# Kernel tuning notes

Measured on AMD Instinct MI355X. Metric: run time of the kernel, lower is better.

Reference implementation:

```python
import jax, jax.numpy as jnp
import numpy as np

N_NODES = 100000
N_EDGES = 6400000
TOKEN_DIM = 16


def setup_inputs() -> dict:
    key = jax.random.key(0)
    k1, k2, k3, k4, k5 = jax.random.split(key, 5)
    x = jax.random.normal(k1, (N_NODES, 1), dtype=jnp.float32)
    edge_index = jax.random.randint(k2, (2, N_EDGES), 0, N_NODES, dtype=jnp.int64)
    # PyTorch nn.Linear init: U(-1/sqrt(fan_in), 1/sqrt(fan_in)); plain normals are fine for a correctness baseline
    w1 = jax.random.normal(k3, (TOKEN_DIM, 2), dtype=jnp.float32) * (1.0 / np.sqrt(2.0))
    b1 = jnp.zeros((TOKEN_DIM,), dtype=jnp.float32)
    w2 = jax.random.normal(k4, (TOKEN_DIM, TOKEN_DIM), dtype=jnp.float32) * (1.0 / np.sqrt(TOKEN_DIM))
    b2 = jnp.zeros((TOKEN_DIM,), dtype=jnp.float32)
    return {"x": x, "edge_index": edge_index, "w1": w1, "b1": b1, "w2": w2, "b2": b2}


def reference(x, edge_index, w1, b1, w2, b2):
    row, col = edge_index[0], edge_index[1]
    # gather-multiply: bond_e = s_row * s_col, shape [E, 1]
    bond = x[row] * x[col]
    # scatter-add into local_field, shape [N, 1]
    local_field = jax.ops.segment_sum(bond, row, num_segments=x.shape[0])
    feats = jnp.concatenate([x, local_field], axis=1)  # [N, 2]
    h = jax.nn.relu(feats @ w1.T + b1)                  # [N, token_dim]
    tokens = jax.nn.relu(h @ w2.T + b2)                 # [N, token_dim]
    return tokens
```

## Files before the change

kernel.cpp:

```cpp
#include <hip/hip_runtime.h>
#include <hip/hip_bf16.h>

#define TOKEN_DIM 16
#define RANGES 5
#define MAX_RS 20000
#define MAX_C  96
#define NXCD   8

__global__ __launch_bounds__(1024, 8)
void nit_phase1(const int* __restrict__ row, const int* __restrict__ col,
                const float* __restrict__ x,
                unsigned short* __restrict__ partial,
                int N, long long E, int chunkE, int RS, int C) {
    __shared__ float acc[MAX_RS];
    const int b = blockIdx.x;
    const int k = b % NXCD;
    const int s = b / NXCD;
    const int r = s % RANGES;
    const int c = k + NXCD * (s / RANGES);
    if (c >= C) return;

    const int base = r * RS;
    int cnt = N - base; if (cnt > RS) cnt = RS; if (cnt < 0) cnt = 0;
    const int t = threadIdx.x, nt = blockDim.x;

    for (int j = t; j < cnt; j += nt) acc[j] = 0.0f;
    __syncthreads();

    long long i0 = (long long)c * chunkE;
    long long i1 = i0 + chunkE; if (i1 > E) i1 = E;
    long long len = (i1 > i0) ? (i1 - i0) : 0;
    long long ngrp = len >> 3;

    long long g = t;
    int4 r0a, r1a, c0a, c1a;
    if (g < ngrp) {
        long long idx = i0 + (g << 3);
        r0a = *reinterpret_cast<const int4*>(row + idx);
        r1a = *reinterpret_cast<const int4*>(row + idx + 4);
        c0a = *reinterpret_cast<const int4*>(col + idx);
        c1a = *reinterpret_cast<const int4*>(col + idx + 4);
    }
    while (g < ngrp) {
        const long long gn = g + nt;
        int4 r0b, r1b, c0b, c1b;
        if (gn < ngrp) {
            long long idx = i0 + (gn << 3);
            r0b = *reinterpret_cast<const int4*>(row + idx);
            r1b = *reinterpret_cast<const int4*>(row + idx + 4);
            c0b = *reinterpret_cast<const int4*>(col + idx);
            c1b = *reinterpret_cast<const int4*>(col + idx + 4);
        }
        unsigned d;
        d = (unsigned)(r0a.x - base); if (d < (unsigned)cnt) atomicAdd(&acc[d], x[c0a.x]);
        d = (unsigned)(r0a.y - base); if (d < (unsigned)cnt) atomicAdd(&acc[d], x[c0a.y]);
        d = (unsigned)(r0a.z - base); if (d < (unsigned)cnt) atomicAdd(&acc[d], x[c0a.z]);
        d = (unsigned)(r0a.w - base); if (d < (unsigned)cnt) atomicAdd(&acc[d], x[c0a.w]);
        d = (unsigned)(r1a.x - base); if (d < (unsigned)cnt) atomicAdd(&acc[d], x[c1a.x]);
        d = (unsigned)(r1a.y - base); if (d < (unsigned)cnt) atomicAdd(&acc[d], x[c1a.y]);
        d = (unsigned)(r1a.z - base); if (d < (unsigned)cnt) atomicAdd(&acc[d], x[c1a.z]);
        d = (unsigned)(r1a.w - base); if (d < (unsigned)cnt) atomicAdd(&acc[d], x[c1a.w]);
        r0a = r0b; r1a = r1b; c0a = c0b; c1a = c1b;
        g = gn;
    }
    for (long long idx = i0 + (ngrp << 3) + t; idx < i1; idx += nt) {
        unsigned d = (unsigned)(row[idx] - base);
        if (d < (unsigned)cnt) atomicAdd(&acc[d], x[col[idx]]);
    }
    __syncthreads();

    unsigned short* dst = partial + (size_t)c * N + base;
    for (int j = t; j < cnt; j += nt) {
        __hip_bfloat16 h = __float2bfloat16(acc[j]);
        __builtin_nontemporal_store(*reinterpret_cast<unsigned short*>(&h), dst + j);
    }
}

__global__ __launch_bounds__(256, 8)
void nit_phase2(const float* __restrict__ x,
                const unsigned short* __restrict__ partial,
                const float* __restrict__ w1, const float* __restrict__ b1,
                const float* __restrict__ w2, const float* __restrict__ b2,
                float* __restrict__ out, int N, int C) {
    __shared__ float sw1[TOKEN_DIM * 2];
    __shared__ float sb1[TOKEN_DIM];
    __shared__ float sw2[TOKEN_DIM * TOKEN_DIM];
    __shared__ float sb2[TOKEN_DIM];
    __shared__ float red[256];

    const int t = threadIdx.x;
    if (t < TOKEN_DIM * TOKEN_DIM) sw2[t] = w2[t];
    if (t < TOKEN_DIM * 2) sw1[t] = w1[t];
    if (t < TOKEN_DIM) { sb1[t] = b1[t]; sb2[t] = b2[t]; }

    const int n = t & 63;
    const int g = t >> 6;
    const int node0 = blockIdx.x * 64;
    const int node = node0 + n;

    float s = 0.0f;
    if (node < N) {
#pragma unroll 4
        for (int c = g; c < C; c += 4) {
            unsigned short u = __builtin_nontemporal_load(partial + (size_t)c * N + node);
            s += __uint_as_float(((unsigned)u) << 16);
        }
    }
    red[t] = s;
    __syncthreads();

    if (t < 64) {
        const int nn = node0 + t;
        if (nn < N) {
            const float ssum = red[t] + red[64 + t] + red[128 + t] + red[192 + t];
            const float xv = x[nn];
            const float lv = xv * ssum;

            float h[TOKEN_DIM];
#pragma unroll
            for (int j = 0; j < TOKEN_DIM; ++j) {
                float v = fmaf(xv, sw1[2 * j], fmaf(lv, sw1[2 * j + 1], sb1[j]));
                h[j] = v > 0.0f ? v : 0.0f;
            }

            float o[TOKEN_DIM];
#pragma unroll
            for (int j = 0; j < TOKEN_DIM; ++j) {
                float v = sb2[j];
#pragma unroll
                for (int k = 0; k < TOKEN_DIM; ++k)
                    v = fmaf(h[k], sw2[j * TOKEN_DIM + k], v);
                o[j] = v > 0.0f ? v : 0.0f;
            }

            float4* op = reinterpret_cast<float4*>(out + (size_t)nn * TOKEN_DIM);
#pragma unroll
            for (int j = 0; j < 4; ++j)
                op[j] = make_float4(o[4 * j], o[4 * j + 1], o[4 * j + 2], o[4 * j + 3]);
        }
    }
}

extern "C" void kernel_launch(void* const* d_in, const int* in_sizes, int n_in,
                              void* d_out, int out_size, void* d_ws, size_t ws_size,
                              hipStream_t stream) {
    const float* x  = (const float*)d_in[0];
    const int*   ei = (const int*)d_in[1];
    const float* w1 = (const float*)d_in[2];
    const float* b1 = (const float*)d_in[3];
    const float* w2 = (const float*)d_in[4];
    const float* b2 = (const float*)d_in[5];
    float* out = (float*)d_out;

    const int N = in_sizes[0];
    const long long E = in_sizes[1] / 2;
    const int* row = ei;
    const int* col = ei + E;

    long long maxC = (long long)(ws_size / ((size_t)N * sizeof(unsigned short)));
    int C = maxC < 1 ? 1 : (maxC > MAX_C ? MAX_C : (int)maxC);
    int RS = ((N + RANGES - 1) / RANGES + 1) & ~1;
    long long ce = (E + C - 1) / C;
    int chunkE = (int)((ce + 7LL) & ~7LL);

    unsigned short* partial = (unsigned short*)d_ws;

    const int cg = (C + NXCD - 1) / NXCD;
    const int grid1 = NXCD * RANGES * cg;
    nit_phase1<<<grid1, 1024, 0, stream>>>(row, col, x, partial,
                                           N, E, chunkE, RS, C);

    int grid2 = (N + 63) / 64;
    nit_phase2<<<grid2, 256, 0, stream>>>(x, partial, w1, b1, w2, b2,
                                          out, N, C);
}
```

Baseline: 154.8 us.

## Batch edge gathers before LDS atomics and vectorize partial-sum traffic

In the scatter kernel, all eight x gathers per edge group are issued first and the LDS atomics come after, separated by a scheduling barrier, so more loads are in flight at once. Partial sums are now packed two bf16 values per 32-bit store instead of one 16-bit nontemporal store each. The reduce/MLP kernel now covers 256 nodes per block: each thread reads four nodes' partials with one 8-byte load, and all 256 threads run the MLP instead of only 64. The trade-offs are higher register pressure from batched gathers, the loss of nontemporal hints, and reliance on N being a multiple of 4 for aligned vector loads.

```diff
diff --git a/kernel.cpp b/kernel.cpp
--- a/kernel.cpp
+++ b/kernel.cpp
@@ -6,6 +6,8 @@
 #define MAX_RS 20000
 #define MAX_C  96
 #define NXCD   8
+
+typedef float floatx4 __attribute__((ext_vector_type(4)));
 
 __global__ __launch_bounds__(1024, 8)
 void nit_phase1(const int* __restrict__ row, const int* __restrict__ col,
@@ -31,6 +33,7 @@
     long long i1 = i0 + chunkE; if (i1 > E) i1 = E;
     long long len = (i1 > i0) ? (i1 - i0) : 0;
     long long ngrp = len >> 3;
+    const unsigned ucnt = (unsigned)cnt;
 
     long long g = t;
     int4 r0a, r1a, c0a, c1a;
@@ -51,28 +54,57 @@
             c0b = *reinterpret_cast<const int4*>(col + idx);
             c1b = *reinterpret_cast<const int4*>(col + idx + 4);
         }
-        unsigned d;
-        d = (unsigned)(r0a.x - base); if (d < (unsigned)cnt) atomicAdd(&acc[d], x[c0a.x]);
-        d = (unsigned)(r0a.y - base); if (d < (unsigned)cnt) atomicAdd(&acc[d], x[c0a.y]);
-        d = (unsigned)(r0a.z - base); if (d < (unsigned)cnt) atomicAdd(&acc[d], x[c0a.z]);
-        d = (unsigned)(r0a.w - base); if (d < (unsigned)cnt) atomicAdd(&acc[d], x[c0a.w]);
-        d = (unsigned)(r1a.x - base); if (d < (unsigned)cnt) atomicAdd(&acc[d], x[c1a.x]);
-        d = (unsigned)(r1a.y - base); if (d < (unsigned)cnt) atomicAdd(&acc[d], x[c1a.y]);
-        d = (unsigned)(r1a.z - base); if (d < (unsigned)cnt) atomicAdd(&acc[d], x[c1a.z]);
-        d = (unsigned)(r1a.w - base); if (d < (unsigned)cnt) atomicAdd(&acc[d], x[c1a.w]);
+        const unsigned d0 = (unsigned)(r0a.x - base);
+        const unsigned d1 = (unsigned)(r0a.y - base);
+        const unsigned d2 = (unsigned)(r0a.z - base);
+        const unsigned d3 = (unsigned)(r0a.w - base);
+        const unsigned d4 = (unsigned)(r1a.x - base);
+        const unsigned d5 = (unsigned)(r1a.y - base);
+        const unsigned d6 = (unsigned)(r1a.z - base);
+        const unsigned d7 = (unsigned)(r1a.w - base);
+
+        float v0, v1, v2, v3, v4, v5, v6, v7;
+        if (d0 < ucnt) v0 = x[c0a.x];
+        if (d1 < ucnt) v1 = x[c0a.y];
+        if (d2 < ucnt) v2 = x[c0a.z];
+        if (d3 < ucnt) v3 = x[c0a.w];
+        if (d4 < ucnt) v4 = x[c1a.x];
+        if (d5 < ucnt) v5 = x[c1a.y];
+        if (d6 < ucnt) v6 = x[c1a.z];
+        if (d7 < ucnt) v7 = x[c1a.w];
+        __builtin_amdgcn_sched_barrier(0);
+
+        if (d0 < ucnt) atomicAdd(&acc[d0], v0);
+        if (d1 < ucnt) atomicAdd(&acc[d1], v1);
+        if (d2 < ucnt) atomicAdd(&acc[d2], v2);
+        if (d3 < ucnt) atomicAdd(&acc[d3], v3);
+        if (d4 < ucnt) atomicAdd(&acc[d4], v4);
+        if (d5 < ucnt) atomicAdd(&acc[d5], v5);
+        if (d6 < ucnt) atomicAdd(&acc[d6], v6);
+        if (d7 < ucnt) atomicAdd(&acc[d7], v7);
+
         r0a = r0b; r1a = r1b; c0a = c0b; c1a = c1b;
         g = gn;
     }
     for (long long idx = i0 + (ngrp << 3) + t; idx < i1; idx += nt) {
         unsigned d = (unsigned)(row[idx] - base);
-        if (d < (unsigned)cnt) atomicAdd(&acc[d], x[col[idx]]);
+        if (d < ucnt) atomicAdd(&acc[d], x[col[idx]]);
     }
     __syncthreads();
 
     unsigned short* dst = partial + (size_t)c * N + base;
-    for (int j = t; j < cnt; j += nt) {
-        __hip_bfloat16 h = __float2bfloat16(acc[j]);
-        __builtin_nontemporal_store(*reinterpret_cast<unsigned short*>(&h), dst + j);
+    unsigned int* dst2 = reinterpret_cast<unsigned int*>(dst);
+    const int cnt2 = cnt >> 1;
+    for (int j = t; j < cnt2; j += nt) {
+        __hip_bfloat16 ha = __float2bfloat16(acc[2 * j]);
+        __hip_bfloat16 hb = __float2bfloat16(acc[2 * j + 1]);
+        unsigned int w = (unsigned int)(*reinterpret_cast<unsigned short*>(&ha))
+                       | ((unsigned int)(*reinterpret_cast<unsigned short*>(&hb)) << 16);
+        dst2[j] = w;
+    }
+    if ((cnt & 1) && t == 0) {
+        __hip_bfloat16 h = __float2bfloat16(acc[cnt - 1]);
+        dst[cnt - 1] = *reinterpret_cast<unsigned short*>(&h);
     }
 }
 
@@ -86,57 +118,69 @@
     __shared__ float sb1[TOKEN_DIM];
     __shared__ float sw2[TOKEN_DIM * TOKEN_DIM];
     __shared__ float sb2[TOKEN_DIM];
-    __shared__ float red[256];
+    __shared__ float red[4][256];
 
     const int t = threadIdx.x;
-    if (t < TOKEN_DIM * TOKEN_DIM) sw2[t] = w2[t];
+    sw2[t] = w2[t];
     if (t < TOKEN_DIM * 2) sw1[t] = w1[t];
     if (t < TOKEN_DIM) { sb1[t] = b1[t]; sb2[t] = b2[t]; }
 
-    const int n = t & 63;
-    const int g = t >> 6;
-    const int node0 = blockIdx.x * 64;
-    const int node = node0 + n;
-
-    float s = 0.0f;
-    if (node < N) {
+    const int lane = t & 63;
+    const int grp  = t >> 6;
+    const int node0 = blockIdx.x << 8;
+    const int n4 = node0 + (lane << 2);
+
+    float s0 = 0.0f, s1 = 0.0f, s2 = 0.0f, s3 = 0.0f;
+    if (n4 + 3 < N) {
+        const unsigned short* p = partial + n4;
 #pragma unroll 4
-        for (int c = g; c < C; c += 4) {
-            unsigned short u = __builtin_nontemporal_load(partial + (size_t)c * N + node);
-            s += __uint_as_float(((unsigned)u) << 16);
-        }
-    }
-    red[t] = s;
+        for (int c = grp; c < C; c += 4) {
+            uint2 u = *reinterpret_cast<const uint2*>(p + (size_t)c * N);
+            s0 += __uint_as_float(u.x << 16);
+            s1 += __uint_as_float(u.x & 0xffff0000u);
+            s2 += __uint_as_float(u.y << 16);
+            s3 += __uint_as_float(u.y & 0xffff0000u);
+        }
+    } else if (n4 < N) {
+        for (int c = grp; c < C; c += 4) {
+            const unsigned short* p = partial + (size_t)c * N;
+            s0 += __uint_as_float(((unsigned)p[n4]) << 16);
+            if (n4 + 1 < N) s1 += __uint_as_float(((unsigned)p[n4 + 1]) << 16);
+            if (n4 + 2 < N) s2 += __uint_as_float(((unsigned)p[n4 + 2]) << 16);
+        }
+    }
+    floatx4 sv = { s0, s1, s2, s3 };
+    *reinterpret_cast<floatx4*>(&red[grp][lane << 2]) = sv;
     __syncthreads();
 
-    if (t < 64) {
-        const int nn = node0 + t;
-        if (nn < N) {
-            const float ssum = red[t] + red[64 + t] + red[128 + t] + red[192 + t];
-            const float xv = x[nn];
-            const float lv = xv * ssum;
-
-            float h[TOKEN_DIM];
-#pragma unroll
-            for (int j = 0; j < TOKEN_DIM; ++j) {
-                float v = fmaf(xv, sw1[2 * j], fmaf(lv, sw1[2 * j + 1], sb1[j]));
-                h[j] = v > 0.0f ? v : 0.0f;
-            }
-
-            float o[TOKEN_DIM];
-#pragma unroll
-            for (int j = 0; j < TOKEN_DIM; ++j) {
-                float v = sb2[j];
-#pragma unroll
-                for (int k = 0; k < TOKEN_DIM; ++k)
-                    v = fmaf(h[k], sw2[j * TOKEN_DIM + k], v);
-                o[j] = v > 0.0f ? v : 0.0f;
-            }
-
-            float4* op = reinterpret_cast<float4*>(out + (size_t)nn * TOKEN_DIM);
-#pragma unroll
-            for (int j = 0; j < 4; ++j)
-                op[j] = make_float4(o[4 * j], o[4 * j + 1], o[4 * j + 2], o[4 * j + 3]);
+    const int n = node0 + t;
+    if (n < N) {
+        const float ssum = red[0][t] + red[1][t] + red[2][t] + red[3][t];
+        const float xv = x[n];
+        const float lv = xv * ssum;
+
+        float h[TOKEN_DIM];
+#pragma unroll
+        for (int j = 0; j < TOKEN_DIM; ++j) {
+            float v = fmaf(xv, sw1[2 * j], fmaf(lv, sw1[2 * j + 1], sb1[j]));
+            h[j] = v > 0.0f ? v : 0.0f;
+        }
+
+        float o[TOKEN_DIM];
+#pragma unroll
+        for (int j = 0; j < TOKEN_DIM; ++j) {
+            float v = sb2[j];
+#pragma unroll
+            for (int kk = 0; kk < TOKEN_DIM; ++kk)
+                v = fmaf(h[kk], sw2[j * TOKEN_DIM + kk], v);
+            o[j] = v > 0.0f ? v : 0.0f;
+        }
+
+        floatx4* op = reinterpret_cast<floatx4*>(out + (size_t)n * TOKEN_DIM);
+#pragma unroll
+        for (int j = 0; j < 4; ++j) {
+            floatx4 w = { o[4 * j], o[4 * j + 1], o[4 * j + 2], o[4 * j + 3] };
+            op[j] = w;
         }
     }
 }
@@ -170,7 +214,7 @@
     nit_phase1<<<grid1, 1024, 0, stream>>>(row, col, x, partial,
                                            N, E, chunkE, RS, C);
 
-    int grid2 = (N + 63) / 64;
+    int grid2 = (N + 255) / 256;
     nit_phase2<<<grid2, 256, 0, stream>>>(x, partial, w1, b1, w2, b2,
                                           out, N, C);
 }
```

Result: faster. 147.2 us (-4.9%).
